# Kernel tuning notes

Hardware: AMD Instinct MI355X
Metric: run time of the kernel (lower is better)

## Reference

```python
import jax, jax.numpy as jnp
import numpy as np

KS = 3          # kernel_size
C_IN = 64       # channel_size
F_OUT = 128     # filters
K_CONNECT = 4   # n_connect (<= KS*KS)
N_POS = KS * KS


def setup_inputs() -> dict:
    key = jax.random.key(0)
    k1, k2, k3, k4 = jax.random.split(key, 4)
    x = jax.random.normal(k1, (16, 128, 128, C_IN), dtype=jnp.float32)
    kern = jax.random.normal(k2, (KS, KS, C_IN, F_OUT), dtype=jnp.float32) * 0.1  # he_uniform-ish
    b = jnp.zeros((F_OUT,), dtype=jnp.float32)
    D = jax.random.normal(k3, (KS, KS, C_IN, F_OUT), dtype=jnp.float32) * 0.5     # trainable logits
    gumbel_u = jax.random.uniform(k4, (1, F_OUT, C_IN, N_POS), dtype=jnp.float32)  # BS=1 uniform noise
    return {"x": x, "kern": kern, "b": b, "D": D, "gumbel_u": gumbel_u}


def dps_topk(D, u, k, temp):
    # D: [KS, KS, C, F]; raw reshape to [F, C, KS*KS] exactly as the TF code does
    F_, C_ = D.shape[3], D.shape[2]
    N_ = D.shape[0] * D.shape[0]
    logits = D.reshape(F_, C_, N_)                       # [F, C, N]
    gn = -0.001 * jnp.log(-jnp.log(u + 1e-20) + 1e-20)   # [1, F, C, N] scaled Gumbel noise
    pert = logits[None] + gn                             # [1, F, C, N]
    # top-k by value (descending), then top-k of the indices -> indices sorted descending
    _, idx = jax.lax.top_k(pert, k)                      # [1, F, C, k] int32
    idx_desc, _ = jax.lax.top_k(idx, k)                  # sorted descending
    topk = idx_desc[..., ::-1]                           # ascending indices
    hard = jax.nn.one_hot(topk, N_, dtype=logits.dtype)  # [1, F, C, k, N]
    cum = jnp.cumsum(hard, axis=-2) - hard               # exclusive cumsum over k (hard is 0/1)
    prob_exp = jnp.exp(logits)[None, :, :, None, :]      # [1, F, C, 1, N] broadcast over k
    soft = jax.nn.softmax(
        (jnp.log(prob_exp * (1.0 - cum + 1e-20)) + gn[:, :, :, None, :]) / temp,
        axis=-1,
    )
    # straight-through: hard forward, soft backward
    return jax.lax.stop_gradient(hard - soft) + soft


def reference(x, kern, b, D, gumbel_u):
    temp = 1.0  # step=0 -> epoch=0 -> initial temperature
    A_ = dps_topk(D, gumbel_u, K_CONNECT, temp)          # [1, F, C, k, N]
    A = A_[0].sum(axis=-2).reshape(KS, KS, C_IN, F_OUT)  # raw reshape, as in the TF code
    # binarize kernel with straight-through estimator
    t1 = jnp.sign(kern)
    t2 = jnp.clip(0.4 * kern, -1.0, 1.0)                 # 2*hard_sigmoid(k) - 1
    ww = jax.lax.stop_gradient(t1 - t2) + t2
    AW = A * ww                                          # sparse-masked binary kernel
    y = jax.lax.conv_general_dilated(
        x, AW, window_strides=(1, 1), padding='SAME',
        dimension_numbers=('NHWC', 'HWIO', 'NHWC'),
    )
    y = y + b
    return jax.nn.relu(y)
```

## Files before the change

### kernel.cpp

```cpp
#include <hip/hip_runtime.h>
#include <hip/hip_bf16.h>
#include <math.h>

#define KS 3
#define C_IN 64
#define F_OUT 128
#define NPOS 9
#define HH 128
#define WWID 128
#define NB 16

typedef __attribute__((ext_vector_type(8))) short bf16x8;
typedef __attribute__((ext_vector_type(4))) float f32x4;

__device__ __forceinline__ unsigned short f2bf(float f) {
  union { float f; unsigned u; } v; v.f = f;
  unsigned u = v.u;
  return (unsigned short)((u + 0x7FFFu + ((u >> 16) & 1u)) >> 16);
}
__device__ __forceinline__ unsigned cvtpk(float lo, float hi) {
  unsigned r;
  asm("v_cvt_pk_bf16_f32 %0, %1, %2" : "=v"(r) : "v"(lo), "v"(hi));
  return r;
}
__device__ __forceinline__ bf16x8 pack8(float4 v0, float4 v1) {
  union { unsigned u[4]; bf16x8 v; } r;
  r.u[0] = cvtpk(v0.x, v0.y); r.u[1] = cvtpk(v0.z, v0.w);
  r.u[2] = cvtpk(v1.x, v1.y); r.u[3] = cvtpk(v1.z, v1.w);
  return r.v;
}

__global__ void compute_aw(const float* __restrict__ kern,
                           const float* __restrict__ D,
                           const float* __restrict__ gu,
                           unsigned short* __restrict__ AWsw) {
  int t = blockIdx.x * blockDim.x + threadIdx.x;
  if (t >= F_OUT * C_IN) return;
  int base = t * NPOS;
  float pert[NPOS];
#pragma unroll
  for (int n = 0; n < NPOS; ++n) {
    float u = gu[base + n];
    float g = -0.001f * logf(-logf(u + 1e-20f) + 1e-20f);
    pert[n] = D[base + n] + g;
  }
  unsigned mask = 0;
#pragma unroll
  for (int k = 0; k < 4; ++k) {
    int best = 0; float bv = -INFINITY;
#pragma unroll
    for (int n = 0; n < NPOS; ++n) {
      bool taken = (mask >> n) & 1;
      if (!taken && pert[n] > bv) { bv = pert[n]; best = n; }
    }
    mask |= (1u << best);
  }
#pragma unroll
  for (int n = 0; n < NPOS; ++n) {
    int L = base + n;
    float kv = kern[L];
    float s = (kv > 0.f) ? 1.f : ((kv < 0.f) ? -1.f : 0.f);
    float v = ((mask >> n) & 1) ? s : 0.f;
    int f = L & (F_OUT - 1);
    int r = L >> 7;
    int c = r & (C_IN - 1);
    int p = r >> 6;
    int ch = c >> 5;
    int cg = (c >> 3) & 3;
    int ps = (cg + ((f & 15) >> 1)) & 3;
    int pg = (p >= 5) ? 1 : 0;
    int pl = p - pg * 5;
    int sl = ch * 2 + pg;
    int off = ((sl * 5 + pl) * F_OUT + f) * 32 + ps * 8 + (c & 7);
    AWsw[off] = f2bf(v);
  }
}

__global__ __launch_bounds__(512, 4)
void conv2(const float* __restrict__ x,
           const unsigned short* __restrict__ AWsw,
           const float* __restrict__ bias,
           float* __restrict__ out) {
  __shared__ __align__(16) unsigned short As[4 * 130 * 32];
  __shared__ __align__(16) unsigned short Bs[5 * F_OUT * 32];

  int tid = threadIdx.x;
  int lane = tid & 63, wave = tid >> 6;
  int lr = lane & 15, lg = lane >> 4;

  int bid = blockIdx.x;
  int wg = (bid & 7) * 128 + (bid >> 3);
  int n = wg >> 6;
  int h0 = (wg & 63) * 2;

  int ms = wave & 3, fh = wave >> 2;
  int ro = ms >> 1;
  int mh = ms & 1;
  int f0 = fh * 64;

  const float* xim = x + ((long long)n * HH) * WWID * C_IN;

#define STAGE_B(SL, NSEG)                                                    \
  {                                                                          \
    const unsigned short* src = AWsw + (SL) * (5 * F_OUT * 32);              \
    _Pragma("unroll")                                                        \
    for (int s = 0; s < (NSEG); ++s) {                                       \
      int ci = s * 512 + tid;                                                \
      *reinterpret_cast<bf16x8*>(Bs + ci * 8) =                              \
          *reinterpret_cast<const bf16x8*>(src + ci * 8);                    \
    }                                                                        \
  }
#define STAGE_A(CH)                                                          \
  {                                                                          \
    _Pragma("unroll")                                                        \
    for (int r = 0; r < 4; ++r) {                                            \
      int hh = h0 - 1 + r;                                                   \
      if ((unsigned)hh < (unsigned)HH) {                                     \
        int px = tid >> 2, cg = tid & 3;                                     \
        const float* sp = xim + (long long)hh * (WWID * C_IN) + px * C_IN +  \
                          (CH) * 32 + cg * 8;                                \
        float4 v0 = *reinterpret_cast<const float4*>(sp);                    \
        float4 v1 = *reinterpret_cast<const float4*>(sp + 4);                \
        int pp = px + 1;                                                     \
        *reinterpret_cast<bf16x8*>(As + r * 4160 + pp * 32 +                 \
                                   (cg ^ (pp & 3)) * 8) = pack8(v0, v1);     \
      }                                                                      \
    }                                                                        \
  }
#define COMPUTE(PG)                                                          \
  {                                                                          \
    _Pragma("unroll")                                                        \
    for (int pl = 0; pl < ((PG) ? 4 : 5); ++pl) {                            \
      int p = (PG) ? pl + 5 : pl;                                            \
      int i = p / 3, j = p % 3;                                              \
      const char* bp = (const char*)Bs + pl * 8192 + (f0 + lr) * 64 +        \
                       (((lg + (lr >> 1)) & 3) << 4);                        \
      bf16x8 b[4];                                                           \
      _Pragma("unroll")                                                      \
      for (int nf = 0; nf < 4; ++nf)                                         \
        b[nf] = *reinterpret_cast<const bf16x8*>(bp + nf * 1024);            \
      bf16x8 a[4];                                                           \
      _Pragma("unroll")                                                      \
      for (int mfi = 0; mfi < 4; ++mfi) {                                    \
        int px = mh * 64 + mfi * 16 + lr + j;                                \
        a[mfi] = *reinterpret_cast<const bf16x8*>(                           \
            (const char*)As + (ro + i) * 8320 + px * 64 +                    \
            ((lg ^ (px & 3)) << 4));                                         \
      }                                                                      \
      _Pragma("unroll")                                                      \
      for (int mfi = 0; mfi < 4; ++mfi)                                      \
        _Pragma("unroll")                                                    \
        for (int nf = 0; nf < 4; ++nf)                                       \
          acc[mfi][nf] = __builtin_amdgcn_mfma_f32_16x16x32_bf16(            \
              a[mfi], b[nf], acc[mfi][nf], 0, 0, 0);                         \
    }                                                                        \
  }

  bf16x8 z = {};
#pragma unroll
  for (int t = 0; t < 5; ++t) {
    int ci = t * 512 + tid;
    if (ci < 2080) *reinterpret_cast<bf16x8*>(As + ci * 8) = z;
  }
  __syncthreads();

  f32x4 acc[4][4] = {};

  STAGE_A(0)
  STAGE_B(0, 5)
  __syncthreads();
  COMPUTE(0)
  __syncthreads();
  STAGE_B(1, 4)
  __syncthreads();
  COMPUTE(1)
  __syncthreads();
  STAGE_A(1)
  STAGE_B(2, 5)
  __syncthreads();
  COMPUTE(0)
  __syncthreads();
  STAGE_B(3, 4)
  __syncthreads();
  COMPUTE(1)

  float bi[4];
#pragma unroll
  for (int nf = 0; nf < 4; ++nf) bi[nf] = bias[f0 + nf * 16 + lr];
  int ho = h0 + ro;
  long long ob = ((long long)(n * HH + ho)) * WWID * F_OUT + f0 + lr;
#pragma unroll
  for (int mfi = 0; mfi < 4; ++mfi) {
#pragma unroll
    for (int r = 0; r < 4; ++r) {
      int w = mh * 64 + mfi * 16 + lg * 4 + r;
      float* op = out + ob + (long long)w * F_OUT;
#pragma unroll
      for (int nf = 0; nf < 4; ++nf)
        op[nf * 16] = fmaxf(acc[mfi][nf][r] + bi[nf], 0.f);
    }
  }
#undef STAGE_B
#undef STAGE_A
#undef COMPUTE
}

extern "C" void kernel_launch(void* const* d_in, const int* in_sizes, int n_in,
                              void* d_out, int out_size, void* d_ws, size_t ws_size,
                              hipStream_t stream) {
  const float* x    = (const float*)d_in[0];
  const float* kern = (const float*)d_in[1];
  const float* bias = (const float*)d_in[2];
  const float* D    = (const float*)d_in[3];
  const float* gu   = (const float*)d_in[4];

  unsigned short* AWsw = (unsigned short*)d_ws;

  compute_aw<<<(F_OUT * C_IN + 255) / 256, 256, 0, stream>>>(kern, D, gu, AWsw);

  conv2<<<NB * (HH / 2), 512, 0, stream>>>(x, AWsw, bias, (float*)d_out);
}
```

Baseline: 68.42 us.

## Process four output rows per 1024-thread block with full-channel weight staging

The conv kernel grows from 2 to 4 output rows per workgroup with 16 waves. Each input halo row is now reused across more outputs, so the halo overhead drops from 4/2 to 6/4 rows per output. All 9 kernel positions for a 32-channel half are staged at once, which cuts the syncs from 7 to 3 but raises LDS use to about 124KB. The A tile uses a new XOR swizzle over 128-byte pairs. Larger blocks and more LDS limit each CU to one block, which may hurt latency hiding.

Result: slower. 89.67 us (+31.1%).

```diff
diff --git a/kernel.cpp b/kernel.cpp
--- a/kernel.cpp
+++ b/kernel.cpp
@@ -68,72 +68,71 @@
     int ch = c >> 5;
     int cg = (c >> 3) & 3;
     int ps = (cg + ((f & 15) >> 1)) & 3;
-    int pg = (p >= 5) ? 1 : 0;
-    int pl = p - pg * 5;
-    int sl = ch * 2 + pg;
-    int off = ((sl * 5 + pl) * F_OUT + f) * 32 + ps * 8 + (c & 7);
+    int off = ((ch * NPOS + p) * F_OUT + f) * 32 + ps * 8 + (c & 7);
     AWsw[off] = f2bf(v);
   }
 }
 
-__global__ __launch_bounds__(512, 4)
-void conv2(const float* __restrict__ x,
+__global__ __launch_bounds__(1024, 4)
+void conv3(const float* __restrict__ x,
            const unsigned short* __restrict__ AWsw,
            const float* __restrict__ bias,
            float* __restrict__ out) {
-  __shared__ __align__(16) unsigned short As[4 * 130 * 32];
-  __shared__ __align__(16) unsigned short Bs[5 * F_OUT * 32];
+  __shared__ __align__(16) unsigned short As[6 * 65 * 64];
+  __shared__ __align__(16) unsigned short Bs[NPOS * F_OUT * 32];
 
   int tid = threadIdx.x;
   int lane = tid & 63, wave = tid >> 6;
   int lr = lane & 15, lg = lane >> 4;
 
   int bid = blockIdx.x;
-  int wg = (bid & 7) * 128 + (bid >> 3);
-  int n = wg >> 6;
-  int h0 = (wg & 63) * 2;
-
-  int ms = wave & 3, fh = wave >> 2;
-  int ro = ms >> 1;
-  int mh = ms & 1;
+  int wg = (bid & 7) * 64 + (bid >> 3);
+  int n = wg >> 5;
+  int h0 = (wg & 31) * 4;
+
+  int mslot = wave & 7, fh = wave >> 3;
+  int ro = mslot >> 1;
+  int px0 = (mslot & 1) * 64;
   int f0 = fh * 64;
 
   const float* xim = x + ((long long)n * HH) * WWID * C_IN;
 
-#define STAGE_B(SL, NSEG)                                                    \
-  {                                                                          \
-    const unsigned short* src = AWsw + (SL) * (5 * F_OUT * 32);              \
-    _Pragma("unroll")                                                        \
-    for (int s = 0; s < (NSEG); ++s) {                                       \
-      int ci = s * 512 + tid;                                                \
-      *reinterpret_cast<bf16x8*>(Bs + ci * 8) =                              \
-          *reinterpret_cast<const bf16x8*>(src + ci * 8);                    \
-    }                                                                        \
-  }
 #define STAGE_A(CH)                                                          \
   {                                                                          \
     _Pragma("unroll")                                                        \
-    for (int r = 0; r < 4; ++r) {                                            \
+    for (int t = 0; t < 3; ++t) {                                            \
+      int ci = t * 1024 + tid;                                               \
+      int r = ci >> 9, px = (ci >> 2) & 127, cg = ci & 3;                    \
       int hh = h0 - 1 + r;                                                   \
       if ((unsigned)hh < (unsigned)HH) {                                     \
-        int px = tid >> 2, cg = tid & 3;                                     \
         const float* sp = xim + (long long)hh * (WWID * C_IN) + px * C_IN +  \
                           (CH) * 32 + cg * 8;                                \
         float4 v0 = *reinterpret_cast<const float4*>(sp);                    \
         float4 v1 = *reinterpret_cast<const float4*>(sp + 4);                \
         int pp = px + 1;                                                     \
-        *reinterpret_cast<bf16x8*>(As + r * 4160 + pp * 32 +                 \
-                                   (cg ^ (pp & 3)) * 8) = pack8(v0, v1);     \
+        int chk = (((pp & 1) << 2) | cg) ^ ((pp >> 1) & 7);                  \
+        *reinterpret_cast<bf16x8*>((char*)As + r * 8320 + (pp >> 1) * 128 +  \
+                                   chk * 16) = pack8(v0, v1);                \
       }                                                                      \
     }                                                                        \
   }
-#define COMPUTE(PG)                                                          \
+#define STAGE_B(CH)                                                          \
+  {                                                                          \
+    const unsigned short* src = AWsw + (CH) * (NPOS * F_OUT * 32);           \
+    _Pragma("unroll")                                                        \
+    for (int t = 0; t < 5; ++t) {                                            \
+      int ci = t * 1024 + tid;                                               \
+      if (ci < 4608)                                                         \
+        *reinterpret_cast<bf16x8*>(Bs + ci * 8) =                            \
+            *reinterpret_cast<const bf16x8*>(src + ci * 8);                  \
+    }                                                                        \
+  }
+#define COMPUTE()                                                            \
   {                                                                          \
     _Pragma("unroll")                                                        \
-    for (int pl = 0; pl < ((PG) ? 4 : 5); ++pl) {                            \
-      int p = (PG) ? pl + 5 : pl;                                            \
-      int i = p / 3, j = p % 3;                                              \
-      const char* bp = (const char*)Bs + pl * 8192 + (f0 + lr) * 64 +        \
+    for (int p = 0; p < NPOS; ++p) {                                         \
+      const int i = p / 3, j = p % 3;                                        \
+      const char* bp = (const char*)Bs + p * 8192 + (f0 + lr) * 64 +         \
                        (((lg + (lr >> 1)) & 3) << 4);                        \
       bf16x8 b[4];                                                           \
       _Pragma("unroll")                                                      \
@@ -142,10 +141,10 @@
       bf16x8 a[4];                                                           \
       _Pragma("unroll")                                                      \
       for (int mfi = 0; mfi < 4; ++mfi) {                                    \
-        int px = mh * 64 + mfi * 16 + lr + j;                                \
+        int pp = px0 + mfi * 16 + lr + j;                                    \
+        int chk = (((pp & 1) << 2) | lg) ^ ((pp >> 1) & 7);                  \
         a[mfi] = *reinterpret_cast<const bf16x8*>(                           \
-            (const char*)As + (ro + i) * 8320 + px * 64 +                    \
-            ((lg ^ (px & 3)) << 4));                                         \
+            (const char*)As + (ro + i) * 8320 + (pp >> 1) * 128 + chk * 16); \
       }                                                                      \
       _Pragma("unroll")                                                      \
       for (int mfi = 0; mfi < 4; ++mfi)                                      \
@@ -158,31 +157,23 @@
 
   bf16x8 z = {};
 #pragma unroll
-  for (int t = 0; t < 5; ++t) {
-    int ci = t * 512 + tid;
-    if (ci < 2080) *reinterpret_cast<bf16x8*>(As + ci * 8) = z;
+  for (int t = 0; t < 4; ++t) {
+    int ci = t * 1024 + tid;
+    if (ci < 3120) *reinterpret_cast<bf16x8*>(As + ci * 8) = z;
   }
   __syncthreads();
 
   f32x4 acc[4][4] = {};
 
   STAGE_A(0)
-  STAGE_B(0, 5)
-  __syncthreads();
-  COMPUTE(0)
-  __syncthreads();
-  STAGE_B(1, 4)
-  __syncthreads();
-  COMPUTE(1)
+  STAGE_B(0)
+  __syncthreads();
+  COMPUTE()
   __syncthreads();
   STAGE_A(1)
-  STAGE_B(2, 5)
-  __syncthreads();
-  COMPUTE(0)
-  __syncthreads();
-  STAGE_B(3, 4)
-  __syncthreads();
-  COMPUTE(1)
+  STAGE_B(1)
+  __syncthreads();
+  COMPUTE()
 
   float bi[4];
 #pragma unroll
@@ -192,16 +183,16 @@
 #pragma unroll
   for (int mfi = 0; mfi < 4; ++mfi) {
 #pragma unroll
-    for (int r = 0; r < 4; ++r) {
-      int w = mh * 64 + mfi * 16 + lg * 4 + r;
+    for (int rr = 0; rr < 4; ++rr) {
+      int w = px0 + mfi * 16 + lg * 4 + rr;
       float* op = out + ob + (long long)w * F_OUT;
 #pragma unroll
       for (int nf = 0; nf < 4; ++nf)
-        op[nf * 16] = fmaxf(acc[mfi][nf][r] + bi[nf], 0.f);
+        op[nf * 16] = fmaxf(acc[mfi][nf][rr] + bi[nf], 0.f);
     }
   }
+#undef STAGE_A
 #undef STAGE_B
-#undef STAGE_A
 #undef COMPUTE
 }
 
@@ -218,5 +209,5 @@
 
   compute_aw<<<(F_OUT * C_IN + 255) / 256, 256, 0, stream>>>(kern, D, gu, AWsw);
 
-  conv2<<<NB * (HH / 2), 512, 0, stream>>>(x, AWsw, bias, (float*)d_out);
-}
+  conv3<<<NB * (HH / 4), 1024, 0, stream>>>(x, AWsw, bias, (float*)d_out);
+}
```
